# Optimization experiments

Measured on AMD Instinct MI355X. Metric: run time of the kernel, lower is better.

The kernel has to match this reference:

```python
import jax, jax.numpy as jnp
import numpy as np

B, L, D_T, DH, ALPHA, DTE, H, NL, DFF = 256, 64, 768, 128, 48, 64, 8, 3, 512


def setup_inputs() -> dict:
    key = jax.random.key(0)
    ks = jax.random.split(key, 24)
    n = lambda i, shape, s=1.0: jax.random.normal(ks[i], shape, dtype=jnp.float32) * s
    return {
        "cls_emb": n(0, (B, L, D_T)),
        "note_times": jnp.sort(jax.random.uniform(ks[1], (B, L), dtype=jnp.float32) * 48.0, axis=-1),
        "note_counts": jax.random.randint(ks[2], (B,), 1, L + 1).astype(jnp.int32),
        "proj_w": n(3, (D_T, DH), D_T ** -0.5), "proj_b": jnp.zeros((DH,), jnp.float32),
        "te_w": n(4, (DTE,)), "te_b": n(5, (DTE,)),
        "wq": n(6, (DTE, DTE), DTE ** -0.5), "wk": n(7, (DTE, DTE), DTE ** -0.5),
        "tf_wq": n(8, (NL, DH, DH), DH ** -0.5), "tf_wk": n(9, (NL, DH, DH), DH ** -0.5),
        "tf_wv": n(10, (NL, DH, DH), DH ** -0.5), "tf_wo": n(11, (NL, DH, DH), DH ** -0.5),
        "tf_ln1_g": jnp.ones((NL, DH), jnp.float32), "tf_ln1_b": jnp.zeros((NL, DH), jnp.float32),
        "tf_w1": n(12, (NL, DH, DFF), DH ** -0.5), "tf_b1": jnp.zeros((NL, DFF), jnp.float32),
        "tf_w2": n(13, (NL, DFF, DH), DFF ** -0.5), "tf_b2": jnp.zeros((NL, DH), jnp.float32),
        "tf_ln2_g": jnp.ones((NL, DH), jnp.float32), "tf_ln2_b": jnp.zeros((NL, DH), jnp.float32),
        "cls_w1": n(14, (DH, DH // 2), DH ** -0.5), "cls_b1": jnp.zeros((DH // 2,), jnp.float32),
        "cls_w2": n(15, (DH // 2, 1), (DH // 2) ** -0.5), "cls_b2": jnp.zeros((1,), jnp.float32),
    }


def _ln(x, g, b):
    mu = x.mean(-1, keepdims=True)
    var = x.var(-1, keepdims=True)
    return (x - mu) * jax.lax.rsqrt(var + 1e-5) * g + b


def _time_embed(t, w, b):
    # mTAND time embedding: dim 0 linear, rest periodic (sin)
    lin = t[..., None] * w + b
    return jnp.concatenate([lin[..., :1], jnp.sin(lin[..., 1:])], axis=-1)


def _forward(cls_emb, note_times, note_counts, proj_w, proj_b, te_w, te_b, wq, wk,
             tf_wq, tf_wk, tf_wv, tf_wo, tf_ln1_g, tf_ln1_b, tf_w1, tf_b1,
             tf_w2, tf_b2, tf_ln2_g, tf_ln2_b, cls_w1, cls_b1, cls_w2, cls_b2):
    # project frozen Longformer CLS embeddings -> note embeddings [B, L, DH]
    note_emb = cls_emb @ proj_w + proj_b
    alpha_pts = jnp.arange(ALPHA, dtype=jnp.float32)
    q_te = _time_embed(alpha_pts, te_w, te_b)          # [A, DTE]
    k_te = _time_embed(note_times, te_w, te_b)         # [B, L, DTE]
    dk = DTE // H
    q = (q_te @ wq).reshape(ALPHA, H, dk)
    k = (k_te @ wk).reshape(B, L, H, dk)
    scores = jnp.einsum('ahd,blhd->bhal', q, k) / np.float32(np.sqrt(dk))
    valid = jnp.arange(L)[None, :] < note_counts[:, None]      # [B, L] ragged mask
    scores = jnp.where(valid[:, None, None, :], scores, jnp.float32(-1e9))
    attn = jax.nn.softmax(scores, axis=-1)                     # [B, H, A, L]
    # one batched interpolation replaces the per-patient / per-dim python loops
    x = jnp.einsum('bhal,blf->bahf', attn, note_emb).mean(axis=2)  # [B, A, DH]
    x = jnp.where((note_counts > 0)[:, None, None], x, 0.0)
    # 3-layer post-norm transformer encoder over the alpha time grid
    hd = DH // H
    for i in range(NL):
        qh = (x @ tf_wq[i]).reshape(B, ALPHA, H, hd)
        kh = (x @ tf_wk[i]).reshape(B, ALPHA, H, hd)
        vh = (x @ tf_wv[i]).reshape(B, ALPHA, H, hd)
        s = jnp.einsum('bqhd,bkhd->bhqk', qh, kh) / np.float32(np.sqrt(hd))
        a = jax.nn.softmax(s, axis=-1)
        o = jnp.einsum('bhqk,bkhd->bqhd', a, vh).reshape(B, ALPHA, DH) @ tf_wo[i]
        x = _ln(x + o, tf_ln1_g[i], tf_ln1_b[i])
        f = jax.nn.relu(x @ tf_w1[i] + tf_b1[i]) @ tf_w2[i] + tf_b2[i]
        x = _ln(x + f, tf_ln2_g[i], tf_ln2_b[i])
    last = x[:, -1, :]
    logits = jax.nn.relu(last @ cls_w1 + cls_b1) @ cls_w2 + cls_b2
    return logits


def reference(cls_emb, note_times, note_counts, proj_w, proj_b, te_w, te_b, wq, wk,
              tf_wq, tf_wk, tf_wv, tf_wo, tf_ln1_g, tf_ln1_b, tf_w1, tf_b1,
              tf_w2, tf_b2, tf_ln2_g, tf_ln2_b, cls_w1, cls_b1, cls_w2, cls_b2):
    return _forward(cls_emb, note_times, note_counts, proj_w, proj_b, te_w, te_b, wq, wk,
                    tf_wq, tf_wk, tf_wv, tf_wo, tf_ln1_g, tf_ln1_b, tf_w1, tf_b1,
                    tf_w2, tf_b2, tf_ln2_g, tf_ln2_b, cls_w1, cls_b1, cls_w2, cls_b2)
```

## Files before the change

kernel.cpp:

```cpp
#include <hip/hip_runtime.h>
#include <hip/hip_bf16.h>

#define B_   256
#define L_   64
#define DT_  768
#define DH_  128
#define AL_  48
#define DTE_ 64
#define H_   8
#define NL_  3
#define DFF_ 512

typedef __attribute__((ext_vector_type(4))) float f32x4;
typedef __attribute__((ext_vector_type(4))) unsigned int u32x4;
typedef __attribute__((ext_vector_type(2))) unsigned int u32x2;
typedef __attribute__((ext_vector_type(8))) short short8;

__device__ inline unsigned short f2bf(float f) {
    union { float f; unsigned u; } v; v.f = f;
    unsigned r = (v.u + 0x7FFFu + ((v.u >> 16) & 1u)) >> 16;
    return (unsigned short)r;
}
__device__ inline unsigned f2bf2(float a, float b) {
    return (unsigned)f2bf(a) | ((unsigned)f2bf(b) << 16);
}
__device__ inline float bf2f(unsigned short u) {
    union { unsigned u; float f; } v; v.u = ((unsigned)u) << 16; return v.f;
}
__device__ inline short8 ldg8(const unsigned short* p) {
    union { short8 s; u32x4 v; } r;
    r.v = *(const u32x4*)p;
    return r.s;
}
__device__ inline unsigned pk_f16(float a, float b) {
    unsigned r;
    asm("v_cvt_pkrtz_f16_f32 %0, %1, %2" : "=v"(r) : "v"(a), "v"(b));
    return r;
}
__device__ inline unsigned pk_max(unsigned a, unsigned b) {
    unsigned r;
    asm("v_pk_max_f16 %0, %1, %2" : "=v"(r) : "v"(a), "v"(b));
    return r;
}
__device__ inline float f16_lo(unsigned h) {
    float f; asm("v_cvt_f32_f16 %0, %1" : "=v"(f) : "v"(h)); return f;
}
__device__ inline float f16_hi(unsigned h) {
    float f; unsigned t = h >> 16;
    asm("v_cvt_f32_f16 %0, %1" : "=v"(f) : "v"(t)); return f;
}

struct TEnt { const float* src; int dstOff; int K; int N; int tile0; };
struct TTab { TEnt e[19]; };

__global__ __launch_bounds__(256) void prep_weights_kernel(TTab tab, unsigned short* __restrict__ wt)
{
    __shared__ unsigned short lds[64][72];
    int ei = 0;
    #pragma unroll
    for (int j = 1; j < 19; ++j) if ((int)blockIdx.x >= tab.e[j].tile0) ei = j;
    TEnt e = tab.e[ei];
    int t = blockIdx.x - e.tile0;
    int tilesK = e.K >> 6;
    int tk = t % tilesK, tn = t / tilesK;
    int tid = threadIdx.x;
    #pragma unroll
    for (int p = 0; p < 16; ++p) {
        int kk = p * 4 + (tid >> 6);
        int n = tid & 63;
        float v = e.src[(size_t)(tk * 64 + kk) * e.N + tn * 64 + n];
        lds[n][kk] = f2bf(v);
    }
    __syncthreads();
    #pragma unroll
    for (int p = 0; p < 2; ++p) {
        int c = p * 256 + tid;
        int n = c >> 3, q = c & 7;
        u32x4 v = *(const u32x4*)(&lds[n][q * 8]);
        *(u32x4*)(&wt[(size_t)e.dstOff + (size_t)(tn * 64 + n) * e.K + tk * 64 + q * 8]) = v;
    }
}

__global__ __launch_bounds__(256) void qk_prep_kernel(
    const float* __restrict__ te_w, const float* __restrict__ te_b,
    const float* __restrict__ wq, float* __restrict__ q_allG)
{
    __shared__ float qte[AL_ * 68];
    int tid = threadIdx.x;
    for (int i = tid; i < AL_ * 64; i += 256) {
        int a = i >> 6, j = i & 63;
        float lin = fmaf((float)a, te_w[j], te_b[j]);
        qte[a * 68 + j] = (j == 0) ? lin : __sinf(lin);
    }
    __syncthreads();
    for (int i = tid; i < AL_ * 64; i += 256) {
        int a = i >> 6, d = i & 63;
        float s0 = 0.f, s1 = 0.f, s2 = 0.f, s3 = 0.f;
        for (int j = 0; j < 64; j += 4) {
            s0 = fmaf(qte[a * 68 + j],     wq[j * 64 + d],       s0);
            s1 = fmaf(qte[a * 68 + j + 1], wq[(j + 1) * 64 + d], s1);
            s2 = fmaf(qte[a * 68 + j + 2], wq[(j + 2) * 64 + d], s2);
            s3 = fmaf(qte[a * 68 + j + 3], wq[(j + 3) * 64 + d], s3);
        }
        q_allG[i] = (s0 + s1) + (s2 + s3);
    }
}

__global__ __launch_bounds__(256) void gemm_proj_kernel(
    const float* __restrict__ A, const unsigned short* __restrict__ Wt,
    const float* __restrict__ bias, unsigned short* __restrict__ C,
    int M, int N, int K)
{
    __shared__ unsigned short As[32 * 64];
    __shared__ unsigned short Bs[128 * 64];
    int tid = threadIdx.x;
    int bm = blockIdx.x * 32;
    int wave = tid >> 6, lane = tid & 63;
    int wm = wave >> 1, wn = wave & 1;
    int g = lane >> 4, r16 = lane & 15;

    f32x4 acc[4] = {};

    for (int k0 = 0; k0 < K; k0 += 64) {
        #pragma unroll
        for (int p = 0; p < 2; ++p) {
            int row = p * 16 + (tid >> 4);
            int c4 = tid & 15;
            f32x4 v = *(const f32x4*)(&A[(size_t)(bm + row) * K + k0 + c4 * 4]);
            u32x2 w;
            w[0] = f2bf2(v[0], v[1]);
            w[1] = f2bf2(v[2], v[3]);
            *(u32x2*)(&As[row * 64 + ((c4 * 4) ^ ((row & 7) << 3))]) = w;
        }
        #pragma unroll
        for (int p = 0; p < 4; ++p) {
            int c = p * 256 + tid;
            int n = c >> 3, q = c & 7;
            u32x4 v = *(const u32x4*)(&Wt[(size_t)n * K + k0 + q * 8]);
            *(u32x4*)(&Bs[n * 64 + ((q * 8) ^ ((n & 7) << 3))]) = v;
        }
        __syncthreads();
        #pragma unroll
        for (int kk = 0; kk < 2; ++kk) {
            short8 af, bf[4];
            int co = kk * 32 + g * 8;
            {
                int row = wm * 16 + r16;
                af = *(const short8*)(&As[row * 64 + (co ^ ((row & 7) << 3))]);
            }
            #pragma unroll
            for (int ni = 0; ni < 4; ++ni) {
                int row = wn * 64 + ni * 16 + r16;
                bf[ni] = *(const short8*)(&Bs[row * 64 + (co ^ ((row & 7) << 3))]);
            }
            #pragma unroll
            for (int ni = 0; ni < 4; ++ni)
                acc[ni] = __builtin_amdgcn_mfma_f32_16x16x32_bf16(af, bf[ni], acc[ni], 0, 0, 0);
        }
        __syncthreads();
    }
    #pragma unroll
    for (int ni = 0; ni < 4; ++ni) {
        int col = wn * 64 + ni * 16 + r16;
        float bv = bias[col];
        #pragma unroll
        for (int r = 0; r < 4; ++r) {
            int row = bm + wm * 16 + g * 4 + r;
            C[(size_t)row * N + col] = f2bf(acc[ni][r] + bv);
        }
    }
}

__global__ __launch_bounds__(256) void first_attn_kernel(
    const float* __restrict__ note_times, const int* __restrict__ note_counts,
    const float* __restrict__ te_w, const float* __restrict__ te_b,
    const float* __restrict__ wk, const float* __restrict__ q_all,
    const unsigned short* __restrict__ note_emb,
    float* __restrict__ x_out, unsigned short* __restrict__ xbf_out)
{
    __shared__ union RU {
        float kkL[64 * 68];
        unsigned short E[32 * 256];
        struct { unsigned short As[32 * 64]; unsigned short Bs[128 * 64]; } mm;
    } ru;
    __shared__ float rsL[32][8];

    const int bx = blockIdx.x;
    const int b = bx >> 1, a0 = (bx & 1) * 24;
    const int tid = threadIdx.x, lane = tid & 63;
    const int wv = __builtin_amdgcn_readfirstlane(tid >> 6);
    const int g = lane >> 4, r16 = lane & 15;
    const int nc = note_counts[b];

    float kte[64];
    {
        float t = note_times[b * 64 + lane];
        #pragma unroll
        for (int j = 0; j < 64; ++j) {
            float lin = fmaf(t, te_w[j], te_b[j]);
            kte[j] = (j == 0) ? lin : __sinf(lin);
        }
    }
    {
        float kvp[16] = {};
        #pragma unroll
        for (int j = 0; j < 64; ++j) {
            #pragma unroll
            for (int dd = 0; dd < 16; ++dd)
                kvp[dd] = fmaf(kte[j], wk[j * 64 + wv * 16 + dd], kvp[dd]);
        }
        #pragma unroll
        for (int q4 = 0; q4 < 4; ++q4)
            *(f32x4*)(&ru.kkL[lane * 68 + wv * 16 + q4 * 4]) = *(const f32x4*)(&kvp[q4 * 4]);
    }
    __syncthreads();
    float kv[64];
    #pragma unroll
    for (int q4 = 0; q4 < 16; ++q4)
        *(f32x4*)(&kv[q4 * 4]) = *(const f32x4*)(&ru.kkL[lane * 68 + q4 * 4]);
    __syncthreads();

    float abar[6] = {};
    const float scale = 0.35355339059327373f;
    #pragma unroll
    for (int p = 0; p < 2; ++p) {
        float e_reg[6][4];
        #pragma unroll
        for (int i = 0; i < 6; ++i) {
            int a = wv * 6 + i;
            float s[4];
            #pragma unroll
            for (int h = 0; h < 4; ++h) {
                float acc = 0.f;
                #pragma unroll
                for (int d = 0; d < 8; ++d)
                    acc = fmaf(q_all[(a0 + a) * 64 + p * 32 + h * 8 + d],
                               kv[p * 32 + h * 8 + d], acc);
                s[h] = (lane < nc) ? acc * scale : -1e9f;
            }
            unsigned m0 = pk_f16(s[0], s[1]);
            unsigned m1 = pk_f16(s[2], s[3]);
            #pragma unroll
            for (int st = 32; st >= 1; st >>= 1) {
                m0 = pk_max(m0, (unsigned)__shfl_xor((int)m0, st));
                m1 = pk_max(m1, (unsigned)__shfl_xor((int)m1, st));
            }
            float mm[4] = { f16_lo(m0), f16_hi(m0), f16_lo(m1), f16_hi(m1) };
            #pragma unroll
            for (int h = 0; h < 4; ++h) {
                float e = __expf(s[h] - mm[h]);
                e_reg[i][h] = e;
                int k = h * 64 + lane;
                ru.E[a * 256 + (k ^ ((a & 7) << 3))] = f2bf(e);
            }
        }
        __syncthreads();
        if (wv < 2) {
            f32x4 acc = {0.f, 0.f, 0.f, 0.f};
            #pragma unroll
            for (int ks = 0; ks < 8; ++ks) {
                int row = wv * 16 + r16;
                short8 af = *(const short8*)(&ru.E[row * 256 + ((ks * 32 + g * 8) ^ ((row & 7) << 3))]);
                short bb = (r16 == (ks >> 1)) ? (short)0x3F80 : (short)0;
                short8 bf = { bb, bb, bb, bb, bb, bb, bb, bb };
                acc = __builtin_amdgcn_mfma_f32_16x16x32_bf16(af, bf, acc, 0, 0, 0);
            }
            if (r16 < 4) {
                #pragma unroll
                for (int r = 0; r < 4; ++r)
                    rsL[wv * 16 + g * 4 + r][p * 4 + r16] = 0.125f / fmaxf(acc[r], 1e-20f);
            }
        }
        __syncthreads();
        #pragma unroll
        for (int i = 0; i < 6; ++i) {
            int a = wv * 6 + i;
            f32x4 rv = *(const f32x4*)(&rsL[a][p * 4]);
            abar[i] = fmaf(e_reg[i][0], rv[0], abar[i]);
            abar[i] = fmaf(e_reg[i][1], rv[1], abar[i]);
            abar[i] = fmaf(e_reg[i][2], rv[2], abar[i]);
            abar[i] = fmaf(e_reg[i][3], rv[3], abar[i]);
        }
    }
    {
        int l = tid & 63;
        #pragma unroll
        for (int pp = 0; pp < 4; ++pp) {
            int c = pp * 4 + (tid >> 6);
            u32x4 v = *(const u32x4*)(&note_emb[((size_t)b * 64 + l) * 128 + c * 8]);
            #pragma unroll
            for (int j = 0; j < 8; ++j) {
                unsigned short h16 = (unsigned short)((j & 1) ? (v[j >> 1] >> 16) : (v[j >> 1] & 0xffff));
                int f = c * 8 + j;
                ru.mm.Bs[f * 64 + (l ^ ((f & 7) << 3))] = h16;
            }
        }
    }
    #pragma unroll
    for (int i = 0; i < 6; ++i) {
        int a = wv * 6 + i;
        ru.mm.As[a * 64 + (lane ^ ((a & 7) << 3))] = f2bf(abar[i]);
    }
    __syncthreads();

    f32x4 pv[4] = {};
    #pragma unroll
    for (int q = 0; q < 4; ++q) {
        int f = wv * 4 + q, mi = f >> 3, ni = f & 7;
        #pragma unroll
        for (int ks = 0; ks < 2; ++ks) {
            int co = ks * 32 + g * 8;
            int raw = mi * 16 + r16, rb = ni * 16 + r16;
            short8 af = *(const short8*)(&ru.mm.As[raw * 64 + (co ^ ((raw & 7) << 3))]);
            short8 bf = *(const short8*)(&ru.mm.Bs[rb * 64 + (co ^ ((rb & 7) << 3))]);
            pv[q] = __builtin_amdgcn_mfma_f32_16x16x32_bf16(af, bf, pv[q], 0, 0, 0);
        }
    }
    #pragma unroll
    for (int q = 0; q < 4; ++q) {
        int f = wv * 4 + q, mi = f >> 3, ni = f & 7;
        #pragma unroll
        for (int r = 0; r < 4; ++r) {
            int row = mi * 16 + g * 4 + r;
            if (row < 24) {
                float v = (nc > 0) ? pv[q][r] : 0.f;
                size_t o = ((size_t)b * AL_ + a0 + row) * 128 + ni * 16 + r16;
                x_out[o] = v;
                xbf_out[o] = f2bf(v);
            }
        }
    }
}

__global__ __launch_bounds__(256) void attn2_kernel(
    const unsigned short* __restrict__ xbf, const unsigned short* __restrict__ WtL,
    unsigned short* __restrict__ o)
{
    __shared__ unsigned short Xs[AL_ * 128];
    __shared__ unsigned short qM[AL_ * 40];
    __shared__ unsigned short kM[AL_ * 40];
    __shared__ unsigned short vT[16 * 72];
    __shared__ float sL[AL_ * 52];
    __shared__ unsigned short P[AL_ * 64];
    int bid = blockIdx.x;
    int b = bid >> 3, h = bid & 7;
    int tid = threadIdx.x, lane = tid & 63;
    int wv = __builtin_amdgcn_readfirstlane(tid >> 6);
    int g = lane >> 4, r16 = lane & 15;

    #pragma unroll
    for (int p = 0; p < 3; ++p) {
        int i = p * 256 + tid;
        int a = i >> 4, c = (i & 15) * 8;
        u32x4 v = *(const u32x4*)(&xbf[((size_t)b * AL_ + a) * 128 + c]);
        *(u32x4*)(&Xs[a * 128 + (c & 64) + ((c & 63) ^ ((a & 7) << 3))]) = v;
    }
    #pragma unroll
    for (int z = 0; z < 3; ++z) {
        int e = z * 256 + tid;
        int a = e >> 4, k2 = 16 + (e & 15);
        qM[a * 40 + k2] = 0;
        kM[a * 40 + k2] = 0;
    }
    { int d = tid >> 4, k2 = 48 + (tid & 15); vT[d * 72 + k2] = 0; }
    __syncthreads();

    if (wv < 3) {
        f32x4 acc[3] = {};
        const unsigned short* Wm = WtL + wv * 16384 + (size_t)(h * 16) * 128;
        #pragma unroll
        for (int kq = 0; kq < 4; ++kq) {
            short8 bf = ldg8(&Wm[(size_t)r16 * 128 + kq * 32 + g * 8]);
            #pragma unroll
            for (int mi = 0; mi < 3; ++mi) {
                int row = mi * 16 + r16;
                int c = kq * 32 + g * 8;
                short8 af = *(const short8*)(&Xs[row * 128 + (c & 64) + ((c & 63) ^ ((row & 7) << 3))]);
                acc[mi] = __builtin_amdgcn_mfma_f32_16x16x32_bf16(af, bf, acc[mi], 0, 0, 0);
            }
        }
        #pragma unroll
        for (int mi = 0; mi < 3; ++mi) {
            #pragma unroll
            for (int r = 0; r < 4; ++r) {
                int a = mi * 16 + g * 4 + r;
                unsigned short hv = f2bf(acc[mi][r]);
                if (wv == 0) qM[a * 40 + r16] = hv;
                else if (wv == 1) kM[a * 40 + r16] = hv;
                else vT[r16 * 72 + a] = hv;
            }
        }
    }
    __syncthreads();

    if (wv < 3) {
        #pragma unroll
        for (int ni = 0; ni < 3; ++ni) {
            f32x4 acc = {0.f, 0.f, 0.f, 0.f};
            short8 af = *(const short8*)(&qM[(wv * 16 + r16) * 40 + g * 8]);
            short8 bf = *(const short8*)(&kM[(ni * 16 + r16) * 40 + g * 8]);
            acc = __builtin_amdgcn_mfma_f32_16x16x32_bf16(af, bf, acc, 0, 0, 0);
            #pragma unroll
            for (int r = 0; r < 4; ++r)
                sL[(wv * 16 + g * 4 + r) * 52 + ni * 16 + r16] = acc[r] * 0.25f;
        }
    }
    __syncthreads();

    if (wv == 0 && lane < 48) {
        float sv[48];
        #pragma unroll
        for (int c4 = 0; c4 < 12; ++c4)
            *(f32x4*)(&sv[c4 * 4]) = *(const f32x4*)(&sL[lane * 52 + c4 * 4]);
        float m = sv[0];
        #pragma unroll
        for (int j = 1; j < 48; ++j) m = fmaxf(m, sv[j]);
        float sum = 0.f;
        #pragma unroll
        for (int j = 0; j < 48; ++j) { sv[j] = __expf(sv[j] - m); sum += sv[j]; }
        float inv = __fdividef(1.f, sum);
        #pragma unroll
        for (int oc = 0; oc < 8; ++oc) {
            u32x4 w = {0u, 0u, 0u, 0u};
            if (oc < 6) {
                w[0] = f2bf2(sv[oc * 8 + 0] * inv, sv[oc * 8 + 1] * inv);
                w[1] = f2bf2(sv[oc * 8 + 2] * inv, sv[oc * 8 + 3] * inv);
                w[2] = f2bf2(sv[oc * 8 + 4] * inv, sv[oc * 8 + 5] * inv);
                w[3] = f2bf2(sv[oc * 8 + 6] * inv, sv[oc * 8 + 7] * inv);
            }
            *(u32x4*)(&P[lane * 64 + ((oc * 8) ^ ((lane & 7) << 3))]) = w;
        }
    }
    __syncthreads();

    if (wv < 3) {
        f32x4 acc = {0.f, 0.f, 0.f, 0.f};
        #pragma unroll
        for (int ks = 0; ks < 2; ++ks) {
            int co = ks * 32 + g * 8;
            int rp = wv * 16 + r16;
            short8 af = *(const short8*)(&P[rp * 64 + (co ^ ((rp & 7) << 3))]);
            short8 bf = *(const short8*)(&vT[r16 * 72 + co]);
            acc = __builtin_amdgcn_mfma_f32_16x16x32_bf16(af, bf, acc, 0, 0, 0);
        }
        #pragma unroll
        for (int r = 0; r < 4; ++r) {
            int a = wv * 16 + g * 4 + r;
            o[((size_t)b * AL_ + a) * 128 + h * 16 + r16] = f2bf(acc[r]);
        }
    }
}

__global__ __launch_bounds__(256) void layer_tail_kernel(
    const unsigned short* __restrict__ obuf, const unsigned short* __restrict__ Wl,
    const float* __restrict__ b1, const float* __restrict__ b2,
    const float* __restrict__ g1, const float* __restrict__ be1,
    const float* __restrict__ g2, const float* __restrict__ be2,
    float* __restrict__ x, unsigned short* __restrict__ xbf)
{
    __shared__ unsigned short OX[16 * 128];
    __shared__ union { unsigned short hid[16 * 512]; float Cs[16 * 132]; } u2;
    __shared__ float xr[16 * 132];
    const int tid = threadIdx.x, lane = tid & 63;
    const int wv = __builtin_amdgcn_readfirstlane(tid >> 6);
    const int g = lane >> 4, r16 = lane & 15;
    const int row0 = blockIdx.x * 16;

    {
        int a = tid >> 4, c = (tid & 15) * 8;
        u32x4 v = *(const u32x4*)(&obuf[(size_t)(row0 + a) * 128 + c]);
        *(u32x4*)(&OX[a * 128 + (c & 64) + ((c & 63) ^ ((a & 7) << 3))]) = v;
    }
    __syncthreads();

    {
        f32x4 wacc[2] = {};
        #pragma unroll
        for (int q = 0; q < 2; ++q) {
            int ni = wv * 2 + q;
            const unsigned short* Wm = Wl + 49152 + (size_t)(ni * 16 + r16) * 128;
            #pragma unroll
            for (int kq = 0; kq < 4; ++kq) {
                int co = kq * 32 + g * 8;
                short8 af = *(const short8*)(&OX[r16 * 128 + (co & 64) + ((co & 63) ^ ((r16 & 7) << 3))]);
                short8 bf = ldg8(Wm + co);
                wacc[q] = __builtin_amdgcn_mfma_f32_16x16x32_bf16(af, bf, wacc[q], 0, 0, 0);
            }
        }
        #pragma unroll
        for (int q = 0; q < 2; ++q) {
            int ni = wv * 2 + q;
            #pragma unroll
            for (int r = 0; r < 4; ++r)
                u2.Cs[(g * 4 + r) * 132 + ni * 16 + r16] = wacc[q][r];
        }
    }
    __syncthreads();

    #pragma unroll
    for (int rr = 0; rr < 4; ++rr) {
        int row = wv * 4 + rr;
        size_t go = (size_t)(row0 + row) * 128;
        float v0 = u2.Cs[row * 132 + lane] + x[go + lane];
        float v1 = u2.Cs[row * 132 + 64 + lane] + x[go + 64 + lane];
        float sum = v0 + v1, sq = v0 * v0 + v1 * v1;
        #pragma unroll
        for (int o2 = 32; o2 >= 1; o2 >>= 1) {
            sum += __shfl_xor(sum, o2);
            sq  += __shfl_xor(sq, o2);
        }
        float mu = sum * (1.f / 128.f);
        float var = sq * (1.f / 128.f) - mu * mu;
        float rs = rsqrtf(var + 1e-5f);
        float o0 = (v0 - mu) * rs * g1[lane] + be1[lane];
        float o1 = (v1 - mu) * rs * g1[lane + 64] + be1[lane + 64];
        xr[row * 132 + lane] = o0;
        xr[row * 132 + 64 + lane] = o1;
        OX[row * 128 + (lane ^ ((row & 7) << 3))] = f2bf(o0);
        OX[row * 128 + 64 + (lane ^ ((row & 7) << 3))] = f2bf(o1);
    }
    __syncthreads();

    {
        f32x4 hacc[8] = {};
        #pragma unroll
        for (int nf = 0; nf < 8; ++nf) {
            int col = wv * 128 + nf * 16 + r16;
            const unsigned short* Wm = Wl + 65536 + (size_t)col * 128;
            #pragma unroll
            for (int kq = 0; kq < 4; ++kq) {
                int co = kq * 32 + g * 8;
                short8 bf = ldg8(Wm + co);
                short8 af = *(const short8*)(&OX[r16 * 128 + (co & 64) + ((co & 63) ^ ((r16 & 7) << 3))]);
                hacc[nf] = __builtin_amdgcn_mfma_f32_16x16x32_bf16(af, bf, hacc[nf], 0, 0, 0);
            }
        }
        #pragma unroll
        for (int nf = 0; nf < 8; ++nf) {
            int col = wv * 128 + nf * 16 + r16;
            float bv = b1[col];
            #pragma unroll
            for (int r = 0; r < 4; ++r) {
                int rowa = g * 4 + r;
                u2.hid[rowa * 512 + (col & 448) + ((col & 63) ^ ((rowa & 7) << 3))] =
                    f2bf(fmaxf(hacc[nf][r] + bv, 0.f));
            }
        }
    }
    __syncthreads();

    f32x4 yacc[2] = {};
    #pragma unroll
    for (int q = 0; q < 2; ++q) {
        int ni = wv * 2 + q;
        const unsigned short* Wm = Wl + 131072 + (size_t)(ni * 16 + r16) * 512;
        #pragma unroll
        for (int kq = 0; kq < 16; ++kq) {
            int co = kq * 32 + g * 8;
            short8 af = *(const short8*)(&u2.hid[r16 * 512 + (co & 448) + ((co & 63) ^ ((r16 & 7) << 3))]);
            short8 bf = ldg8(Wm + co);
            yacc[q] = __builtin_amdgcn_mfma_f32_16x16x32_bf16(af, bf, yacc[q], 0, 0, 0);
        }
    }
    __syncthreads();
    #pragma unroll
    for (int q = 0; q < 2; ++q) {
        int ni = wv * 2 + q;
        float bv = b2[ni * 16 + r16];
        #pragma unroll
        for (int r = 0; r < 4; ++r)
            u2.Cs[(g * 4 + r) * 132 + ni * 16 + r16] = yacc[q][r] + bv;
    }
    __syncthreads();

    #pragma unroll
    for (int rr = 0; rr < 4; ++rr) {
        int row = wv * 4 + rr;
        size_t go = (size_t)(row0 + row) * 128;
        float v0 = u2.Cs[row * 132 + lane] + xr[row * 132 + lane];
        float v1 = u2.Cs[row * 132 + 64 + lane] + xr[row * 132 + 64 + lane];
        float sum = v0 + v1, sq = v0 * v0 + v1 * v1;
        #pragma unroll
        for (int o2 = 32; o2 >= 1; o2 >>= 1) {
            sum += __shfl_xor(sum, o2);
            sq  += __shfl_xor(sq, o2);
        }
        float mu = sum * (1.f / 128.f);
        float var = sq * (1.f / 128.f) - mu * mu;
        float rs = rsqrtf(var + 1e-5f);
        float o0 = (v0 - mu) * rs * g2[lane] + be2[lane];
        float o1 = (v1 - mu) * rs * g2[lane + 64] + be2[lane + 64];
        x[go + lane] = o0;
        x[go + 64 + lane] = o1;
        xbf[go + lane] = f2bf(o0);
        xbf[go + 64 + lane] = f2bf(o1);
    }
}

__global__ __launch_bounds__(64) void head_kernel(
    const float* __restrict__ x, const float* __restrict__ w1,
    const float* __restrict__ b1, const float* __restrict__ w2,
    const float* __restrict__ b2, float* __restrict__ out)
{
    int b = blockIdx.x;
    int j = threadIdx.x;
    const float* xr = x + ((size_t)b * AL_ + (AL_ - 1)) * DH_;
    float hj = b1[j];
    for (int d = 0; d < DH_; ++d) hj = fmaf(xr[d], w1[d * 64 + j], hj);
    hj = fmaxf(hj, 0.f);
    float acc = hj * w2[j];
    #pragma unroll
    for (int d = 32; d >= 1; d >>= 1) acc += __shfl_xor(acc, d);
    if (j == 0) out[b] = acc + b2[0];
}

extern "C" void kernel_launch(void* const* d_in, const int* in_sizes, int n_in,
                              void* d_out, int out_size, void* d_ws, size_t ws_size,
                              hipStream_t stream) {
    (void)in_sizes; (void)n_in; (void)out_size; (void)ws_size;
    const float* cls_emb    = (const float*)d_in[0];
    const float* note_times = (const float*)d_in[1];
    const int*   note_counts= (const int*)d_in[2];
    const float* proj_w     = (const float*)d_in[3];
    const float* proj_b     = (const float*)d_in[4];
    const float* te_w       = (const float*)d_in[5];
    const float* te_b       = (const float*)d_in[6];
    const float* wq         = (const float*)d_in[7];
    const float* wk         = (const float*)d_in[8];
    const float* tf_wq      = (const float*)d_in[9];
    const float* tf_wk      = (const float*)d_in[10];
    const float* tf_wv      = (const float*)d_in[11];
    const float* tf_wo      = (const float*)d_in[12];
    const float* tf_ln1_g   = (const float*)d_in[13];
    const float* tf_ln1_b   = (const float*)d_in[14];
    const float* tf_w1      = (const float*)d_in[15];
    const float* tf_b1      = (const float*)d_in[16];
    const float* tf_w2      = (const float*)d_in[17];
    const float* tf_b2      = (const float*)d_in[18];
    const float* tf_ln2_g   = (const float*)d_in[19];
    const float* tf_ln2_b   = (const float*)d_in[20];
    const float* cls_w1     = (const float*)d_in[21];
    const float* cls_b1     = (const float*)d_in[22];
    const float* cls_w2     = (const float*)d_in[23];
    const float* cls_b2     = (const float*)d_in[24];
    float* out = (float*)d_out;
    float* ws = (float*)d_ws;

    unsigned short* note_emb16 = (unsigned short*)(ws + 0);
    float* x        = ws + 1048576;
    unsigned short* obuf16 = (unsigned short*)(ws + 2621440);
    unsigned short* xbf    = (unsigned short*)(ws + 3407872);
    float* q_all    = ws + 4194304;
    unsigned short* wt     = (unsigned short*)(ws + 4197376);

    TTab tab;
    int tile = 0, idx = 0;
    auto add = [&](const float* src, int dstOff, int K, int N) {
        tab.e[idx].src = src; tab.e[idx].dstOff = dstOff;
        tab.e[idx].K = K; tab.e[idx].N = N; tab.e[idx].tile0 = tile;
        tile += (K / 64) * (N / 64); ++idx;
    };
    add(proj_w, 0, DT_, DH_);
    int layerBase[NL_];
    for (int i = 0; i < NL_; ++i) {
        int base = 98304 + i * 196608;
        layerBase[i] = base;
        add(tf_wq + (size_t)i * DH_ * DH_, base,           DH_, DH_);
        add(tf_wk + (size_t)i * DH_ * DH_, base + 16384,   DH_, DH_);
        add(tf_wv + (size_t)i * DH_ * DH_, base + 32768,   DH_, DH_);
        add(tf_wo + (size_t)i * DH_ * DH_, base + 49152,   DH_, DH_);
        add(tf_w1 + (size_t)i * DH_ * DFF_, base + 65536,  DH_, DFF_);
        add(tf_w2 + (size_t)i * DFF_ * DH_, base + 131072, DFF_, DH_);
    }
    prep_weights_kernel<<<tile, 256, 0, stream>>>(tab, wt);
    qk_prep_kernel<<<1, 256, 0, stream>>>(te_w, te_b, wq, q_all);

    const int Mx = B_ * AL_;

    gemm_proj_kernel<<<(B_ * L_) / 32, 256, 0, stream>>>(
        cls_emb, wt, proj_b, note_emb16, B_ * L_, DH_, DT_);

    first_attn_kernel<<<B_ * 2, 256, 0, stream>>>(
        note_times, note_counts, te_w, te_b, wk, q_all, note_emb16, x, xbf);

    for (int i = 0; i < NL_; ++i) {
        int base = layerBase[i];
        attn2_kernel<<<B_ * H_, 256, 0, stream>>>(xbf, wt + base, obuf16);
        layer_tail_kernel<<<Mx / 16, 256, 0, stream>>>(
            obuf16, wt + base,
            tf_b1 + i * DFF_, tf_b2 + i * DH_,
            tf_ln1_g + i * DH_, tf_ln1_b + i * DH_,
            tf_ln2_g + i * DH_, tf_ln2_b + i * DH_,
            x, xbf);
    }

    head_kernel<<<B_, 64, 0, stream>>>(x, cls_w1, cls_b1, cls_w2, cls_b2, out);
}
```

Measured before the change: 204.1 us.

## Fuse qk prep and head into other kernels, prune last layer rows, shrink attn block

Merges the query time-embedding prep into the weight-prep launch as an extra block, and folds the classifier head into the last layer-tail kernel. In the final layer that kernel processes only the last 16 rows per batch element, since only the final position feeds the head. The attention kernel drops its idle fourth wave and spreads softmax across three waves with shuffle reductions instead of one wave doing it serially. This removes launches and unused final-layer work, but relies on the final-layer row pruning being exact and on xr being valid shared scratch.

```diff
diff --git a/kernel.cpp b/kernel.cpp
--- a/kernel.cpp
+++ b/kernel.cpp
@@ -53,9 +53,34 @@
 struct TEnt { const float* src; int dstOff; int K; int N; int tile0; };
 struct TTab { TEnt e[19]; };
 
-__global__ __launch_bounds__(256) void prep_weights_kernel(TTab tab, unsigned short* __restrict__ wt)
+__global__ __launch_bounds__(256) void prep_weights_kernel(
+    TTab tab, int ntile, unsigned short* __restrict__ wt,
+    const float* __restrict__ te_w, const float* __restrict__ te_b,
+    const float* __restrict__ wq, float* __restrict__ q_allG)
 {
     __shared__ unsigned short lds[64][72];
+    __shared__ float qte[AL_ * 68];
+    int tid = threadIdx.x;
+    if ((int)blockIdx.x >= ntile) {
+        for (int i = tid; i < AL_ * 64; i += 256) {
+            int a = i >> 6, j = i & 63;
+            float lin = fmaf((float)a, te_w[j], te_b[j]);
+            qte[a * 68 + j] = (j == 0) ? lin : __sinf(lin);
+        }
+        __syncthreads();
+        for (int i = tid; i < AL_ * 64; i += 256) {
+            int a = i >> 6, d = i & 63;
+            float s0 = 0.f, s1 = 0.f, s2 = 0.f, s3 = 0.f;
+            for (int j = 0; j < 64; j += 4) {
+                s0 = fmaf(qte[a * 68 + j],     wq[j * 64 + d],       s0);
+                s1 = fmaf(qte[a * 68 + j + 1], wq[(j + 1) * 64 + d], s1);
+                s2 = fmaf(qte[a * 68 + j + 2], wq[(j + 2) * 64 + d], s2);
+                s3 = fmaf(qte[a * 68 + j + 3], wq[(j + 3) * 64 + d], s3);
+            }
+            q_allG[i] = (s0 + s1) + (s2 + s3);
+        }
+        return;
+    }
     int ei = 0;
     #pragma unroll
     for (int j = 1; j < 19; ++j) if ((int)blockIdx.x >= tab.e[j].tile0) ei = j;
@@ -63,7 +88,6 @@
     int t = blockIdx.x - e.tile0;
     int tilesK = e.K >> 6;
     int tk = t % tilesK, tn = t / tilesK;
-    int tid = threadIdx.x;
     #pragma unroll
     for (int p = 0; p < 16; ++p) {
         int kk = p * 4 + (tid >> 6);
@@ -78,31 +102,6 @@
         int n = c >> 3, q = c & 7;
         u32x4 v = *(const u32x4*)(&lds[n][q * 8]);
         *(u32x4*)(&wt[(size_t)e.dstOff + (size_t)(tn * 64 + n) * e.K + tk * 64 + q * 8]) = v;
-    }
-}
-
-__global__ __launch_bounds__(256) void qk_prep_kernel(
-    const float* __restrict__ te_w, const float* __restrict__ te_b,
-    const float* __restrict__ wq, float* __restrict__ q_allG)
-{
-    __shared__ float qte[AL_ * 68];
-    int tid = threadIdx.x;
-    for (int i = tid; i < AL_ * 64; i += 256) {
-        int a = i >> 6, j = i & 63;
-        float lin = fmaf((float)a, te_w[j], te_b[j]);
-        qte[a * 68 + j] = (j == 0) ? lin : __sinf(lin);
-    }
-    __syncthreads();
-    for (int i = tid; i < AL_ * 64; i += 256) {
-        int a = i >> 6, d = i & 63;
-        float s0 = 0.f, s1 = 0.f, s2 = 0.f, s3 = 0.f;
-        for (int j = 0; j < 64; j += 4) {
-            s0 = fmaf(qte[a * 68 + j],     wq[j * 64 + d],       s0);
-            s1 = fmaf(qte[a * 68 + j + 1], wq[(j + 1) * 64 + d], s1);
-            s2 = fmaf(qte[a * 68 + j + 2], wq[(j + 2) * 64 + d], s2);
-            s3 = fmaf(qte[a * 68 + j + 3], wq[(j + 3) * 64 + d], s3);
-        }
-        q_allG[i] = (s0 + s1) + (s2 + s3);
     }
 }
 
@@ -332,7 +331,7 @@
     }
 }
 
-__global__ __launch_bounds__(256) void attn2_kernel(
+__global__ __launch_bounds__(192) void attn2_kernel(
     const unsigned short* __restrict__ xbf, const unsigned short* __restrict__ WtL,
     unsigned short* __restrict__ o)
 {
@@ -349,23 +348,28 @@
     int g = lane >> 4, r16 = lane & 15;
 
     #pragma unroll
-    for (int p = 0; p < 3; ++p) {
-        int i = p * 256 + tid;
+    for (int p = 0; p < 4; ++p) {
+        int i = p * 192 + tid;
         int a = i >> 4, c = (i & 15) * 8;
         u32x4 v = *(const u32x4*)(&xbf[((size_t)b * AL_ + a) * 128 + c]);
         *(u32x4*)(&Xs[a * 128 + (c & 64) + ((c & 63) ^ ((a & 7) << 3))]) = v;
     }
-    #pragma unroll
-    for (int z = 0; z < 3; ++z) {
-        int e = z * 256 + tid;
-        int a = e >> 4, k2 = 16 + (e & 15);
+    for (int i = tid; i < 768; i += 192) {
+        int a = i >> 4, k2 = 16 + (i & 15);
         qM[a * 40 + k2] = 0;
         kM[a * 40 + k2] = 0;
     }
-    { int d = tid >> 4, k2 = 48 + (tid & 15); vT[d * 72 + k2] = 0; }
-    __syncthreads();
-
-    if (wv < 3) {
+    for (int i = tid; i < 256; i += 192) {
+        int d = i >> 4, k2 = 48 + (i & 15);
+        vT[d * 72 + k2] = 0;
+    }
+    for (int i = tid; i < 768; i += 192) {
+        int a = i >> 4, c = 48 + (i & 15);
+        P[a * 64 + (c ^ ((a & 7) << 3))] = 0;
+    }
+    __syncthreads();
+
+    {
         f32x4 acc[3] = {};
         const unsigned short* Wm = WtL + wv * 16384 + (size_t)(h * 16) * 128;
         #pragma unroll
@@ -393,7 +397,7 @@
     }
     __syncthreads();
 
-    if (wv < 3) {
+    {
         #pragma unroll
         for (int ni = 0; ni < 3; ++ni) {
             f32x4 acc = {0.f, 0.f, 0.f, 0.f};
@@ -407,33 +411,41 @@
     }
     __syncthreads();
 
-    if (wv == 0 && lane < 48) {
-        float sv[48];
-        #pragma unroll
-        for (int c4 = 0; c4 < 12; ++c4)
-            *(f32x4*)(&sv[c4 * 4]) = *(const f32x4*)(&sL[lane * 52 + c4 * 4]);
-        float m = sv[0];
-        #pragma unroll
-        for (int j = 1; j < 48; ++j) m = fmaxf(m, sv[j]);
+    {
+        int row = wv * 16 + (lane >> 2), sub = lane & 3;
+        f32x4 v0 = *(const f32x4*)(&sL[row * 52 + sub * 4]);
+        f32x4 v1 = *(const f32x4*)(&sL[row * 52 + 16 + sub * 4]);
+        f32x4 v2 = *(const f32x4*)(&sL[row * 52 + 32 + sub * 4]);
+        float m = fmaxf(fmaxf(fmaxf(v0[0], v0[1]), fmaxf(v0[2], v0[3])),
+                        fmaxf(fmaxf(v1[0], v1[1]), fmaxf(v1[2], v1[3])));
+        m = fmaxf(m, fmaxf(fmaxf(v2[0], v2[1]), fmaxf(v2[2], v2[3])));
+        m = fmaxf(m, __shfl_xor(m, 1));
+        m = fmaxf(m, __shfl_xor(m, 2));
+        float e[12];
+        #pragma unroll
+        for (int j = 0; j < 4; ++j) {
+            e[j]     = __expf(v0[j] - m);
+            e[4 + j] = __expf(v1[j] - m);
+            e[8 + j] = __expf(v2[j] - m);
+        }
         float sum = 0.f;
         #pragma unroll
-        for (int j = 0; j < 48; ++j) { sv[j] = __expf(sv[j] - m); sum += sv[j]; }
+        for (int j = 0; j < 12; ++j) sum += e[j];
+        sum += __shfl_xor(sum, 1);
+        sum += __shfl_xor(sum, 2);
         float inv = __fdividef(1.f, sum);
         #pragma unroll
-        for (int oc = 0; oc < 8; ++oc) {
-            u32x4 w = {0u, 0u, 0u, 0u};
-            if (oc < 6) {
-                w[0] = f2bf2(sv[oc * 8 + 0] * inv, sv[oc * 8 + 1] * inv);
-                w[1] = f2bf2(sv[oc * 8 + 2] * inv, sv[oc * 8 + 3] * inv);
-                w[2] = f2bf2(sv[oc * 8 + 4] * inv, sv[oc * 8 + 5] * inv);
-                w[3] = f2bf2(sv[oc * 8 + 6] * inv, sv[oc * 8 + 7] * inv);
-            }
-            *(u32x4*)(&P[lane * 64 + ((oc * 8) ^ ((lane & 7) << 3))]) = w;
-        }
-    }
-    __syncthreads();
-
-    if (wv < 3) {
+        for (int c = 0; c < 3; ++c) {
+            u32x2 w;
+            w[0] = f2bf2(e[c * 4 + 0] * inv, e[c * 4 + 1] * inv);
+            w[1] = f2bf2(e[c * 4 + 2] * inv, e[c * 4 + 3] * inv);
+            int col = c * 16 + sub * 4;
+            *(u32x2*)(&P[row * 64 + (col ^ ((row & 7) << 3))]) = w;
+        }
+    }
+    __syncthreads();
+
+    {
         f32x4 acc = {0.f, 0.f, 0.f, 0.f};
         #pragma unroll
         for (int ks = 0; ks < 2; ++ks) {
@@ -456,7 +468,10 @@
     const float* __restrict__ b1, const float* __restrict__ b2,
     const float* __restrict__ g1, const float* __restrict__ be1,
     const float* __restrict__ g2, const float* __restrict__ be2,
-    float* __restrict__ x, unsigned short* __restrict__ xbf)
+    float* __restrict__ x, unsigned short* __restrict__ xbf,
+    int last, const float* __restrict__ cw1, const float* __restrict__ cb1,
+    const float* __restrict__ cw2, const float* __restrict__ cb2,
+    float* __restrict__ outp)
 {
     __shared__ unsigned short OX[16 * 128];
     __shared__ union { unsigned short hid[16 * 512]; float Cs[16 * 132]; } u2;
@@ -464,7 +479,7 @@
     const int tid = threadIdx.x, lane = tid & 63;
     const int wv = __builtin_amdgcn_readfirstlane(tid >> 6);
     const int g = lane >> 4, r16 = lane & 15;
-    const int row0 = blockIdx.x * 16;
+    const int row0 = last ? ((int)blockIdx.x * 48 + 32) : ((int)blockIdx.x * 16);
 
     {
         int a = tid >> 4, c = (tid & 15) * 8;
@@ -590,28 +605,30 @@
         float rs = rsqrtf(var + 1e-5f);
         float o0 = (v0 - mu) * rs * g2[lane] + be2[lane];
         float o1 = (v1 - mu) * rs * g2[lane + 64] + be2[lane + 64];
-        x[go + lane] = o0;
-        x[go + 64 + lane] = o1;
-        xbf[go + lane] = f2bf(o0);
-        xbf[go + 64 + lane] = f2bf(o1);
-    }
-}
-
-__global__ __launch_bounds__(64) void head_kernel(
-    const float* __restrict__ x, const float* __restrict__ w1,
-    const float* __restrict__ b1, const float* __restrict__ w2,
-    const float* __restrict__ b2, float* __restrict__ out)
-{
-    int b = blockIdx.x;
-    int j = threadIdx.x;
-    const float* xr = x + ((size_t)b * AL_ + (AL_ - 1)) * DH_;
-    float hj = b1[j];
-    for (int d = 0; d < DH_; ++d) hj = fmaf(xr[d], w1[d * 64 + j], hj);
-    hj = fmaxf(hj, 0.f);
-    float acc = hj * w2[j];
-    #pragma unroll
-    for (int d = 32; d >= 1; d >>= 1) acc += __shfl_xor(acc, d);
-    if (j == 0) out[b] = acc + b2[0];
+        if (!last) {
+            x[go + lane] = o0;
+            x[go + 64 + lane] = o1;
+            xbf[go + lane] = f2bf(o0);
+            xbf[go + 64 + lane] = f2bf(o1);
+        } else {
+            xr[row * 132 + lane] = o0;
+            xr[row * 132 + 64 + lane] = o1;
+        }
+    }
+    if (last) {
+        __syncthreads();
+        if (wv == 0) {
+            float hj = cb1[lane];
+            #pragma unroll 8
+            for (int d = 0; d < 128; ++d)
+                hj = fmaf(xr[15 * 132 + d], cw1[d * 64 + lane], hj);
+            hj = fmaxf(hj, 0.f);
+            float acc = hj * cw2[lane];
+            #pragma unroll
+            for (int o2 = 32; o2 >= 1; o2 >>= 1) acc += __shfl_xor(acc, o2);
+            if (lane == 0) outp[blockIdx.x] = acc + cb2[0];
+        }
+    }
 }
 
 extern "C" void kernel_launch(void* const* d_in, const int* in_sizes, int n_in,
@@ -672,8 +689,7 @@
         add(tf_w1 + (size_t)i * DH_ * DFF_, base + 65536,  DH_, DFF_);
         add(tf_w2 + (size_t)i * DFF_ * DH_, base + 131072, DFF_, DH_);
     }
-    prep_weights_kernel<<<tile, 256, 0, stream>>>(tab, wt);
-    qk_prep_kernel<<<1, 256, 0, stream>>>(te_w, te_b, wq, q_all);
+    prep_weights_kernel<<<tile + 1, 256, 0, stream>>>(tab, tile, wt, te_w, te_b, wq, q_all);
 
     const int Mx = B_ * AL_;
 
@@ -685,14 +701,14 @@
 
     for (int i = 0; i < NL_; ++i) {
         int base = layerBase[i];
-        attn2_kernel<<<B_ * H_, 256, 0, stream>>>(xbf, wt + base, obuf16);
-        layer_tail_kernel<<<Mx / 16, 256, 0, stream>>>(
+        int last = (i == NL_ - 1);
+        attn2_kernel<<<B_ * H_, 192, 0, stream>>>(xbf, wt + base, obuf16);
+        layer_tail_kernel<<<last ? B_ : (Mx / 16), 256, 0, stream>>>(
             obuf16, wt + base,
             tf_b1 + i * DFF_, tf_b2 + i * DH_,
             tf_ln1_g + i * DH_, tf_ln1_b + i * DH_,
             tf_ln2_g + i * DH_, tf_ln2_b + i * DH_,
-            x, xbf);
-    }
-
-    head_kernel<<<B_, 64, 0, stream>>>(x, cls_w1, cls_b1, cls_w2, cls_b2, out);
-}
+            x, xbf,
+            last, cls_w1, cls_b1, cls_w2, cls_b2, out);
+    }
+}
```

After: 187.5 us. -8.1%, faster.
